# Optimization experiments

Measured on AMD Instinct MI355X. Metric: run time of the kernel, lower is better.

The kernel has to match this reference:

```python
import jax, jax.numpy as jnp
import numpy as np

EMB_DIM = 1024
N_HEADS = 16
HEAD_DIM = EMB_DIM // N_HEADS


def setup_inputs() -> dict:
    key = jax.random.key(0)
    ks = jax.random.split(key, 6)
    B, T, C = 2, 2048, EMB_DIM
    s = 1.0 / np.sqrt(C)
    return {
        "x": jax.random.normal(ks[0], (B, T, C), dtype=jnp.float32),
        "W_query": jax.random.normal(ks[1], (C, C), dtype=jnp.float32) * s,
        "W_key": jax.random.normal(ks[2], (C, C), dtype=jnp.float32) * s,
        "W_value": jax.random.normal(ks[3], (C, C), dtype=jnp.float32) * s,
        "W_out": jax.random.normal(ks[4], (C, C), dtype=jnp.float32) * s,
        "b_out": jax.random.normal(ks[5], (C,), dtype=jnp.float32) * 0.01,
    }


def reference(x, W_query, W_key, W_value, W_out, b_out):
    # x: [B, T, C]. Linear weights stored as [in, out] (transposed torch layout).
    B, T, C = x.shape
    H, D = N_HEADS, HEAD_DIM

    def split_heads(t):  # [B,T,C] -> [B,H,T,D]
        return t.reshape(B, T, H, D).transpose(0, 2, 1, 3)

    q = split_heads(x @ W_query)
    k = split_heads(x @ W_key)
    v = split_heads(x @ W_value)

    scale = 1.0 / jnp.sqrt(jnp.asarray(D, dtype=x.dtype))
    att = jnp.einsum("bhqd,bhkd->bhqk", q, k) * scale  # [B,H,T,T]
    causal = jnp.tril(jnp.ones((T, T), dtype=bool))
    att = jnp.where(causal[None, None], att, jnp.asarray(-jnp.inf, dtype=att.dtype))
    att = jax.nn.softmax(att, axis=-1)
    # dropout is identity in eval / drop_rate=0
    y = jnp.einsum("bhqk,bhkd->bhqd", att, v)  # [B,H,T,D]
    y = y.transpose(0, 2, 1, 3).reshape(B, T, C)
    return y @ W_out + b_out
```

## Files before the change

kernel.cpp:

```cpp
#include <hip/hip_runtime.h>
#include <hip/hip_bf16.h>
#include <math.h>

#define Bsz 2
#define Tsz 2048
#define Csz 1024
#define Hsz 16
#define Dsz 64

typedef __attribute__((ext_vector_type(8))) short frag8;
typedef __attribute__((ext_vector_type(4))) float f4;
typedef __attribute__((ext_vector_type(8))) unsigned short us8;

static __device__ __forceinline__ unsigned short f2bf(float f) {
  union { __hip_bfloat16 h; unsigned short u; } c;
  c.h = __float2bfloat16(f);
  return c.u;
}

#define GLDS16(g, l)                                                        \
  __builtin_amdgcn_global_load_lds(                                         \
      (const __attribute__((address_space(1))) void*)(g),                   \
      (__attribute__((address_space(3))) void*)(l), 16, 0, 0)

__global__ __launch_bounds__(256) void cast_x(const float* __restrict__ x,
                                              unsigned short* __restrict__ xb) {
  const int i = (blockIdx.x * 256 + threadIdx.x) * 8;
  const float4 a = *(const float4*)(x + i);
  const float4 b = *(const float4*)(x + i + 4);
  us8 v;
  v[0] = f2bf(a.x); v[1] = f2bf(a.y); v[2] = f2bf(a.z); v[3] = f2bf(a.w);
  v[4] = f2bf(b.x); v[5] = f2bf(b.y); v[6] = f2bf(b.z); v[7] = f2bf(b.w);
  *(us8*)(xb + i) = v;
}

__global__ __launch_bounds__(256) void transpose_cast(
    const float* __restrict__ s0, const float* __restrict__ s1,
    const float* __restrict__ s2, const float* __restrict__ s3,
    unsigned short* __restrict__ d0, unsigned short* __restrict__ d1,
    unsigned short* __restrict__ d2, unsigned short* __restrict__ d3) {
  __shared__ float Ls[64][65];
  const int mat = blockIdx.x >> 8;
  const int tile = blockIdx.x & 255;
  const float* src = mat == 0 ? s0 : mat == 1 ? s1 : mat == 2 ? s2 : s3;
  unsigned short* dst = mat == 0 ? d0 : mat == 1 ? d1 : mat == 2 ? d2 : d3;
  const int tr0 = (tile >> 4) << 6, tc0 = (tile & 15) << 6;
  const int t = threadIdx.x;
  const int lr = t >> 4, lc = (t & 15) << 2;
#pragma unroll
  for (int j = 0; j < 4; ++j) {
    const float4 v = *(const float4*)(src + (size_t)(tr0 + lr + j * 16) * 1024 + tc0 + lc);
    Ls[lr + j * 16][lc + 0] = v.x;
    Ls[lr + j * 16][lc + 1] = v.y;
    Ls[lr + j * 16][lc + 2] = v.z;
    Ls[lr + j * 16][lc + 3] = v.w;
  }
  __syncthreads();
#pragma unroll
  for (int j = 0; j < 4; ++j) {
    ushort4 v;
    v.x = f2bf(Ls[lc + 0][lr + j * 16]);
    v.y = f2bf(Ls[lc + 1][lr + j * 16]);
    v.z = f2bf(Ls[lc + 2][lr + j * 16]);
    v.w = f2bf(Ls[lc + 3][lr + j * 16]);
    *(ushort4*)(dst + (size_t)(tc0 + lr + j * 16) * 1024 + tr0 + lc) = v;
  }
}

template <int MODE>
__global__ __launch_bounds__(256) void mm_bt(
    const unsigned short* __restrict__ A, const unsigned short* __restrict__ Bt,
    const float* __restrict__ bias, unsigned short* __restrict__ O0,
    unsigned short* __restrict__ O1, unsigned short* __restrict__ O2,
    float* __restrict__ Of) {
  __shared__ __align__(16) unsigned short As[128 * 32];
  __shared__ __align__(16) unsigned short Bs[128 * 32];
  const int K = 1024;
  const int tid = threadIdx.x;
  const int wave = tid >> 6, lane = tid & 63;
  const int quad = lane >> 4, l16 = lane & 15;
  const int wm = wave >> 1, wn = wave & 1;
  const int row0 = blockIdx.y << 7, col0 = blockIdx.x << 7;

  const int sr = lane >> 2, sg = lane & 3;
  const int rA0 = wave * 32 + sr;
  const int g0 = sg ^ ((rA0 >> 1) & 3);
  const unsigned short* gA0 = A + (size_t)(row0 + rA0) * K + (g0 << 3);
  const unsigned short* gA1 = gA0 + (size_t)16 * K;
  const unsigned short* gB0 = Bt + (size_t)(col0 + rA0) * K + (g0 << 3);
  const unsigned short* gB1 = gB0 + (size_t)16 * K;
  unsigned short* lA0 = &As[(wave * 32) * 32];
  unsigned short* lA1 = &As[(wave * 32 + 16) * 32];
  unsigned short* lB0 = &Bs[(wave * 32) * 32];
  unsigned short* lB1 = &Bs[(wave * 32 + 16) * 32];

  f4 acc[4][4];
#pragma unroll
  for (int i = 0; i < 4; ++i)
#pragma unroll
    for (int j = 0; j < 4; ++j) acc[i][j] = (f4){0.f, 0.f, 0.f, 0.f};

  for (int kk = 0; kk < K; kk += 32) {
    __syncthreads();
    GLDS16(gA0 + kk, lA0);
    GLDS16(gA1 + kk, lA1);
    GLDS16(gB0 + kk, lB0);
    GLDS16(gB1 + kk, lB1);
    __syncthreads();

    frag8 af[4], bf[4];
#pragma unroll
    for (int mt = 0; mt < 4; ++mt) {
      const int r = wm * 64 + mt * 16 + l16;
      af[mt] = *(const frag8*)&As[r * 32 + ((quad ^ ((r >> 1) & 3)) << 3)];
    }
#pragma unroll
    for (int nt = 0; nt < 4; ++nt) {
      const int n = wn * 64 + nt * 16 + l16;
      bf[nt] = *(const frag8*)&Bs[n * 32 + ((quad ^ ((n >> 1) & 3)) << 3)];
    }
#pragma unroll
    for (int mt = 0; mt < 4; ++mt)
#pragma unroll
      for (int nt = 0; nt < 4; ++nt)
        acc[mt][nt] = __builtin_amdgcn_mfma_f32_16x16x32_bf16(af[mt], bf[nt], acc[mt][nt], 0, 0, 0);
  }

  if (MODE == 0) {
    if (col0 < 2048) {
      const bool isK = (col0 >= 1024);
      unsigned short* dst = isK ? O1 : O0;
      const float sc = isK ? 1.0f : 0.125f;
#pragma unroll
      for (int mt = 0; mt < 4; ++mt)
#pragma unroll
        for (int nt = 0; nt < 4; ++nt) {
          const int m = row0 + wm * 64 + mt * 16 + quad * 4;
          const int n = (col0 & 1023) + wn * 64 + nt * 16 + l16;
          const int b = m >> 11, h = n >> 6, d = n & 63;
#pragma unroll
          for (int r = 0; r < 4; ++r) {
            const int tk = (m + r) & (Tsz - 1);
            dst[(((size_t)b * Hsz + h) * Tsz + tk) * Dsz + d] = f2bf(acc[mt][nt][r] * sc);
          }
        }
    } else {
#pragma unroll
      for (int mt = 0; mt < 4; ++mt)
#pragma unroll
        for (int nt = 0; nt < 4; ++nt) {
          const int tok = row0 + wm * 64 + mt * 16 + quad * 4;
          const int ch = (col0 - 2048) + wn * 64 + nt * 16 + l16;
          const int b = tok >> 11, tk = tok & (Tsz - 1);
          const int h = ch >> 6, d = ch & 63;
          ushort4 v;
          v.x = f2bf(acc[mt][nt][0]); v.y = f2bf(acc[mt][nt][1]);
          v.z = f2bf(acc[mt][nt][2]); v.w = f2bf(acc[mt][nt][3]);
          *(ushort4*)&O2[(((size_t)b * Hsz + h) * Dsz + d) * Tsz + tk] = v;
        }
    }
  } else {
#pragma unroll
    for (int mt = 0; mt < 4; ++mt)
#pragma unroll
      for (int nt = 0; nt < 4; ++nt) {
        const int m = row0 + wm * 64 + mt * 16 + quad * 4;
        const int n = col0 + wn * 64 + nt * 16 + l16;
        const float bv = bias[n];
#pragma unroll
        for (int r = 0; r < 4; ++r)
          Of[(size_t)(m + r) * Csz + n] = acc[mt][nt][r] + bv;
      }
  }
}

#define PST 40
__global__ __launch_bounds__(256, 4) void attn_mfma(
    const unsigned short* __restrict__ Qb,
    const unsigned short* __restrict__ Kb,
    const unsigned short* __restrict__ VTb,
    unsigned short* __restrict__ Y) {
  __shared__ __align__(16) unsigned short Ks[2][2048];
  __shared__ __align__(16) unsigned short Vs[2][2048];
  __shared__ __align__(16) unsigned short Pb[4][16 * PST];

  const int tid = threadIdx.x;
  const int wave = tid >> 6, lane = tid & 63;
  const int quad = lane >> 4, l16 = lane & 15;

  const int bh = blockIdx.x >> 5;
  int qt = blockIdx.x & 31;
  if (bh >= 16) qt = 31 - qt;
  const int qb_w = (qt << 6) + wave * 16;

  const unsigned short* Qh = Qb + (size_t)bh * Tsz * Dsz;
  const unsigned short* Kh = Kb + (size_t)bh * Tsz * Dsz;
  const unsigned short* Vh = VTb + (size_t)bh * Dsz * Tsz;

  const int kkey = tid >> 3, kc = tid & 7;
  const int vd = tid >> 2, vc = tid & 3;
  const unsigned short* gK = Kh + (size_t)kkey * Dsz + ((kc ^ (kkey & 7)) << 3);
  const unsigned short* gV = Vh + (size_t)vd * Tsz + ((vc ^ ((vd + (vd >> 2)) & 3)) << 3);

  frag8 qf[2];
  qf[0] = *(const frag8*)(Qh + (size_t)(qb_w + l16) * Dsz + quad * 8);
  qf[1] = *(const frag8*)(Qh + (size_t)(qb_w + l16) * Dsz + 32 + quad * 8);

  f4 o[4];
  o[0] = o[1] = o[2] = o[3] = (f4){0.f, 0.f, 0.f, 0.f};
  float lsum = 0.f;
  const f4 zf = (f4){0.f, 0.f, 0.f, 0.f};
  unsigned short* Pw = &Pb[wave][0];
  const int fl = (l16 + (l16 >> 2)) & 3;
  const int kend_w = qb_w + 16;
  const int nch = 2 * qt + 2;

  GLDS16(gK, &Ks[0][wave * 512]);
  GLDS16(gV, &Vs[0][wave * 512]);
  GLDS16(gK + 32 * Dsz, &Ks[1][wave * 512]);
  GLDS16(gV + 32, &Vs[1][wave * 512]);
  __syncthreads();

  for (int i = 0; i < nch; ++i) {
    const int k0 = i << 5;
    const int bsel = i & 1;
    if (k0 < kend_w) {
      frag8 kf[2][2], vf[4];
#pragma unroll
      for (int n = 0; n < 2; ++n)
#pragma unroll
        for (int ks = 0; ks < 2; ++ks)
          kf[n][ks] = *(const frag8*)&Ks[bsel][(n * 16 + l16) * 64 + (((ks * 4 + quad) ^ (l16 & 7)) << 3)];
#pragma unroll
      for (int nt = 0; nt < 4; ++nt)
        vf[nt] = *(const frag8*)&Vs[bsel][(nt * 16 + l16) * 32 + ((quad ^ fl) << 3)];

      f4 st[2];
#pragma unroll
      for (int n = 0; n < 2; ++n) {
        f4 a = __builtin_amdgcn_mfma_f32_16x16x32_bf16(kf[n][0], qf[0], zf, 0, 0, 0);
        st[n] = __builtin_amdgcn_mfma_f32_16x16x32_bf16(kf[n][1], qf[1], a, 0, 0, 0);
      }

      const bool domask = (k0 + 31 > qb_w);
#pragma unroll
      for (int n = 0; n < 2; ++n) {
        const int key0 = k0 + n * 16 + quad * 4;
        ushort4 pk;
        float p0, p1, p2, p3;
        {
          float sv = st[n][0];
          if (domask && (key0 + 0 > qb_w + l16)) sv = -INFINITY;
          p0 = __expf(sv);
        }
        {
          float sv = st[n][1];
          if (domask && (key0 + 1 > qb_w + l16)) sv = -INFINITY;
          p1 = __expf(sv);
        }
        {
          float sv = st[n][2];
          if (domask && (key0 + 2 > qb_w + l16)) sv = -INFINITY;
          p2 = __expf(sv);
        }
        {
          float sv = st[n][3];
          if (domask && (key0 + 3 > qb_w + l16)) sv = -INFINITY;
          p3 = __expf(sv);
        }
        lsum += (p0 + p1) + (p2 + p3);
        pk.x = f2bf(p0); pk.y = f2bf(p1); pk.z = f2bf(p2); pk.w = f2bf(p3);
        *(ushort4*)&Pw[l16 * PST + n * 16 + quad * 4] = pk;
      }

      const frag8 pf = *(const frag8*)&Pw[l16 * PST + quad * 8];
#pragma unroll
      for (int nt = 0; nt < 4; ++nt)
        o[nt] = __builtin_amdgcn_mfma_f32_16x16x32_bf16(pf, vf[nt], o[nt], 0, 0, 0);
    }
    __syncthreads();
    if (i + 2 < nch) {
      GLDS16(gK + (size_t)(k0 + 64) * Dsz, &Ks[bsel][wave * 512]);
      GLDS16(gV + (k0 + 64), &Vs[bsel][wave * 512]);
    }
  }

  lsum += __shfl_xor(lsum, 16);
  lsum += __shfl_xor(lsum, 32);

  const int b = bh >> 4, h = bh & 15;
#pragma unroll
  for (int r = 0; r < 4; ++r) {
    const float inv = 1.f / __shfl(lsum, quad * 4 + r);
    const int t = qb_w + quad * 4 + r;
    unsigned short* yp = Y + ((size_t)b * Tsz + t) * Csz + h * 64 + l16;
#pragma unroll
    for (int nt = 0; nt < 4; ++nt)
      yp[nt * 16] = f2bf(o[nt][r] * inv);
  }
}

extern "C" void kernel_launch(void* const* d_in, const int* in_sizes, int n_in,
                              void* d_out, int out_size, void* d_ws, size_t ws_size,
                              hipStream_t stream) {
  const float* x  = (const float*)d_in[0];
  const float* Wq = (const float*)d_in[1];
  const float* Wk = (const float*)d_in[2];
  const float* Wv = (const float*)d_in[3];
  const float* Wo = (const float*)d_in[4];
  const float* bo = (const float*)d_in[5];

  const size_t NEL = (size_t)Bsz * Tsz * Csz;
  const size_t WSZ = (size_t)Csz * Csz;
  unsigned short* xb  = (unsigned short*)d_ws;
  unsigned short* WT  = xb + NEL;
  unsigned short* WoT = WT + 3 * WSZ;
  unsigned short* Qb  = WoT + WSZ;
  unsigned short* Kb  = Qb + NEL;
  unsigned short* VTb = Kb + NEL;
  unsigned short* Yb  = VTb + NEL;

  cast_x<<<NEL / 2048, 256, 0, stream>>>(x, xb);
  transpose_cast<<<1024, 256, 0, stream>>>(Wq, Wk, Wv, Wo,
                                           WT, WT + WSZ, WT + 2 * WSZ, WoT);

  mm_bt<0><<<dim3(24, 32), 256, 0, stream>>>(xb, WT, nullptr, Qb, Kb, VTb, nullptr);

  attn_mfma<<<Bsz * Hsz * (Tsz / 64), 256, 0, stream>>>(Qb, Kb, VTb, Yb);

  mm_bt<2><<<dim3(8, 32), 256, 0, stream>>>(Yb, WoT, bo, nullptr, nullptr, nullptr,
                                            (float*)d_out);
}
```

Baseline: 196.9 us.

## Retile GEMMs to K=64, widen attention to 32 rows per wave, fp16 PV via registers

The GEMM now stages K=64 slices with an 8-way XOR swizzle, and is templated on M tile so the output projection uses 64-row tiles for more blocks. Attention now handles 128 queries per block and 32 per wave, which reuses each K/V chunk across two query subtiles. It folds log2(e) into the Q scale and uses exp2, and stores V and P as fp16. When the 16x16x16 f16 MFMA is available, P feeds the PV MFMA straight from registers with no LDS round trip. Costs are higher register pressure, occupancy hint dropped to 2, fewer attention blocks, and fp16 range risk for V.

```diff
diff --git a/kernel.cpp b/kernel.cpp
--- a/kernel.cpp
+++ b/kernel.cpp
@@ -11,17 +11,30 @@
 typedef __attribute__((ext_vector_type(8))) short frag8;
 typedef __attribute__((ext_vector_type(4))) float f4;
 typedef __attribute__((ext_vector_type(8))) unsigned short us8;
+typedef __attribute__((ext_vector_type(4))) _Float16 frag4h;
+typedef __attribute__((ext_vector_type(8))) _Float16 frag8h;
+
+#if __has_builtin(__builtin_amdgcn_mfma_f32_16x16x16f16)
+#define PV_DIRECT 1
+#endif
 
 static __device__ __forceinline__ unsigned short f2bf(float f) {
   union { __hip_bfloat16 h; unsigned short u; } c;
   c.h = __float2bfloat16(f);
   return c.u;
 }
+static __device__ __forceinline__ unsigned short f2h(float f) {
+  union { _Float16 h; unsigned short u; } c;
+  c.h = (_Float16)f;
+  return c.u;
+}
 
 #define GLDS16(g, l)                                                        \
   __builtin_amdgcn_global_load_lds(                                         \
       (const __attribute__((address_space(1))) void*)(g),                   \
       (__attribute__((address_space(3))) void*)(l), 16, 0, 0)
+
+#define QSCALE 0.18033688f
 
 __global__ __launch_bounds__(256) void cast_x(const float* __restrict__ x,
                                               unsigned short* __restrict__ xb) {
@@ -67,75 +80,73 @@
   }
 }
 
-template <int MODE>
+template <int MODE, int MT>
 __global__ __launch_bounds__(256) void mm_bt(
     const unsigned short* __restrict__ A, const unsigned short* __restrict__ Bt,
     const float* __restrict__ bias, unsigned short* __restrict__ O0,
     unsigned short* __restrict__ O1, unsigned short* __restrict__ O2,
     float* __restrict__ Of) {
-  __shared__ __align__(16) unsigned short As[128 * 32];
-  __shared__ __align__(16) unsigned short Bs[128 * 32];
+  __shared__ __align__(16) unsigned short As[MT * 32 * 64];
+  __shared__ __align__(16) unsigned short Bs[128 * 64];
   const int K = 1024;
   const int tid = threadIdx.x;
   const int wave = tid >> 6, lane = tid & 63;
   const int quad = lane >> 4, l16 = lane & 15;
-  const int wm = wave >> 1, wn = wave & 1;
-  const int row0 = blockIdx.y << 7, col0 = blockIdx.x << 7;
-
-  const int sr = lane >> 2, sg = lane & 3;
-  const int rA0 = wave * 32 + sr;
-  const int g0 = sg ^ ((rA0 >> 1) & 3);
-  const unsigned short* gA0 = A + (size_t)(row0 + rA0) * K + (g0 << 3);
-  const unsigned short* gA1 = gA0 + (size_t)16 * K;
-  const unsigned short* gB0 = Bt + (size_t)(col0 + rA0) * K + (g0 << 3);
-  const unsigned short* gB1 = gB0 + (size_t)16 * K;
-  unsigned short* lA0 = &As[(wave * 32) * 32];
-  unsigned short* lA1 = &As[(wave * 32 + 16) * 32];
-  unsigned short* lB0 = &Bs[(wave * 32) * 32];
-  unsigned short* lB1 = &Bs[(wave * 32 + 16) * 32];
-
-  f4 acc[4][4];
-#pragma unroll
-  for (int i = 0; i < 4; ++i)
+  const int wrow = (wave >> 1) * (MT * 16), wn = wave & 1;
+  const int row0 = blockIdx.y * (MT * 32), col0 = blockIdx.x << 7;
+
+  const int sr = lane >> 3, sg = lane & 7;
+  const int g0 = sg ^ sr;
+  const unsigned short* gA = A + (size_t)(row0 + wave * (MT * 8) + sr) * K + (g0 << 3);
+  const unsigned short* gB = Bt + (size_t)(col0 + wave * 32 + sr) * K + (g0 << 3);
+
+  f4 acc[MT][4];
+#pragma unroll
+  for (int i = 0; i < MT; ++i)
 #pragma unroll
     for (int j = 0; j < 4; ++j) acc[i][j] = (f4){0.f, 0.f, 0.f, 0.f};
 
-  for (int kk = 0; kk < K; kk += 32) {
+  for (int kk = 0; kk < K; kk += 64) {
     __syncthreads();
-    GLDS16(gA0 + kk, lA0);
-    GLDS16(gA1 + kk, lA1);
-    GLDS16(gB0 + kk, lB0);
-    GLDS16(gB1 + kk, lB1);
+#pragma unroll
+    for (int s = 0; s < MT; ++s)
+      GLDS16(gA + kk + (size_t)(s * 8) * K, &As[(wave * (MT * 8) + s * 8) * 64]);
+#pragma unroll
+    for (int s = 0; s < 4; ++s)
+      GLDS16(gB + kk + (size_t)(s * 8) * K, &Bs[(wave * 32 + s * 8) * 64]);
     __syncthreads();
 
-    frag8 af[4], bf[4];
-#pragma unroll
-    for (int mt = 0; mt < 4; ++mt) {
-      const int r = wm * 64 + mt * 16 + l16;
-      af[mt] = *(const frag8*)&As[r * 32 + ((quad ^ ((r >> 1) & 3)) << 3)];
-    }
-#pragma unroll
-    for (int nt = 0; nt < 4; ++nt) {
-      const int n = wn * 64 + nt * 16 + l16;
-      bf[nt] = *(const frag8*)&Bs[n * 32 + ((quad ^ ((n >> 1) & 3)) << 3)];
-    }
-#pragma unroll
-    for (int mt = 0; mt < 4; ++mt)
-#pragma unroll
-      for (int nt = 0; nt < 4; ++nt)
-        acc[mt][nt] = __builtin_amdgcn_mfma_f32_16x16x32_bf16(af[mt], bf[nt], acc[mt][nt], 0, 0, 0);
+#pragma unroll
+    for (int ks = 0; ks < 2; ++ks) {
+      frag8 af[MT], bf[4];
+#pragma unroll
+      for (int mt = 0; mt < MT; ++mt) {
+        const int r = wrow + mt * 16 + l16;
+        af[mt] = *(const frag8*)&As[r * 64 + (((ks * 4 + quad) ^ (l16 & 7)) << 3)];
+      }
+#pragma unroll
+      for (int nt = 0; nt < 4; ++nt) {
+        const int n = wn * 64 + nt * 16 + l16;
+        bf[nt] = *(const frag8*)&Bs[n * 64 + (((ks * 4 + quad) ^ (l16 & 7)) << 3)];
+      }
+#pragma unroll
+      for (int mt = 0; mt < MT; ++mt)
+#pragma unroll
+        for (int nt = 0; nt < 4; ++nt)
+          acc[mt][nt] = __builtin_amdgcn_mfma_f32_16x16x32_bf16(af[mt], bf[nt], acc[mt][nt], 0, 0, 0);
+    }
   }
 
   if (MODE == 0) {
     if (col0 < 2048) {
       const bool isK = (col0 >= 1024);
       unsigned short* dst = isK ? O1 : O0;
-      const float sc = isK ? 1.0f : 0.125f;
-#pragma unroll
-      for (int mt = 0; mt < 4; ++mt)
+      const float sc = isK ? 1.0f : QSCALE;
+#pragma unroll
+      for (int mt = 0; mt < MT; ++mt)
 #pragma unroll
         for (int nt = 0; nt < 4; ++nt) {
-          const int m = row0 + wm * 64 + mt * 16 + quad * 4;
+          const int m = row0 + wrow + mt * 16 + quad * 4;
           const int n = (col0 & 1023) + wn * 64 + nt * 16 + l16;
           const int b = m >> 11, h = n >> 6, d = n & 63;
 #pragma unroll
@@ -146,25 +157,25 @@
         }
     } else {
 #pragma unroll
-      for (int mt = 0; mt < 4; ++mt)
+      for (int mt = 0; mt < MT; ++mt)
 #pragma unroll
         for (int nt = 0; nt < 4; ++nt) {
-          const int tok = row0 + wm * 64 + mt * 16 + quad * 4;
+          const int tok = row0 + wrow + mt * 16 + quad * 4;
           const int ch = (col0 - 2048) + wn * 64 + nt * 16 + l16;
           const int b = tok >> 11, tk = tok & (Tsz - 1);
           const int h = ch >> 6, d = ch & 63;
           ushort4 v;
-          v.x = f2bf(acc[mt][nt][0]); v.y = f2bf(acc[mt][nt][1]);
-          v.z = f2bf(acc[mt][nt][2]); v.w = f2bf(acc[mt][nt][3]);
+          v.x = f2h(acc[mt][nt][0]); v.y = f2h(acc[mt][nt][1]);
+          v.z = f2h(acc[mt][nt][2]); v.w = f2h(acc[mt][nt][3]);
           *(ushort4*)&O2[(((size_t)b * Hsz + h) * Dsz + d) * Tsz + tk] = v;
         }
     }
   } else {
 #pragma unroll
-    for (int mt = 0; mt < 4; ++mt)
+    for (int mt = 0; mt < MT; ++mt)
 #pragma unroll
       for (int nt = 0; nt < 4; ++nt) {
-        const int m = row0 + wm * 64 + mt * 16 + quad * 4;
+        const int m = row0 + wrow + mt * 16 + quad * 4;
         const int n = col0 + wn * 64 + nt * 16 + l16;
         const float bv = bias[n];
 #pragma unroll
@@ -174,24 +185,25 @@
   }
 }
 
-#define PST 40
-__global__ __launch_bounds__(256, 4) void attn_mfma(
+__global__ __launch_bounds__(256, 2) void attn_mfma(
     const unsigned short* __restrict__ Qb,
     const unsigned short* __restrict__ Kb,
     const unsigned short* __restrict__ VTb,
     unsigned short* __restrict__ Y) {
   __shared__ __align__(16) unsigned short Ks[2][2048];
   __shared__ __align__(16) unsigned short Vs[2][2048];
-  __shared__ __align__(16) unsigned short Pb[4][16 * PST];
-
+#ifndef PV_DIRECT
+  __shared__ __align__(16) unsigned short Pb[4][32 * 72];
+#endif
   const int tid = threadIdx.x;
   const int wave = tid >> 6, lane = tid & 63;
   const int quad = lane >> 4, l16 = lane & 15;
 
-  const int bh = blockIdx.x >> 5;
-  int qt = blockIdx.x & 31;
-  if (bh >= 16) qt = 31 - qt;
-  const int qb_w = (qt << 6) + wave * 16;
+  const int bh = blockIdx.x >> 4;
+  const int qtr = blockIdx.x & 15;
+  const int qt = (bh < 16) ? (15 - qtr) : qtr;
+  const int qb0 = qt << 7;
+  const int qb_w = qb0 + wave * 32;
 
   const unsigned short* Qh = Qb + (size_t)bh * Tsz * Dsz;
   const unsigned short* Kh = Kb + (size_t)bh * Tsz * Dsz;
@@ -202,22 +214,28 @@
   const unsigned short* gK = Kh + (size_t)kkey * Dsz + ((kc ^ (kkey & 7)) << 3);
   const unsigned short* gV = Vh + (size_t)vd * Tsz + ((vc ^ ((vd + (vd >> 2)) & 3)) << 3);
 
-  frag8 qf[2];
-  qf[0] = *(const frag8*)(Qh + (size_t)(qb_w + l16) * Dsz + quad * 8);
-  qf[1] = *(const frag8*)(Qh + (size_t)(qb_w + l16) * Dsz + 32 + quad * 8);
-
-  f4 o[4];
-  o[0] = o[1] = o[2] = o[3] = (f4){0.f, 0.f, 0.f, 0.f};
-  float lsum = 0.f;
+  frag8 qf[2][2];
+#pragma unroll
+  for (int m = 0; m < 2; ++m)
+#pragma unroll
+    for (int ks = 0; ks < 2; ++ks)
+      qf[m][ks] = *(const frag8*)(Qh + (size_t)(qb_w + m * 16 + l16) * Dsz + ks * 32 + quad * 8);
+
+  f4 o[2][4];
+  float lsum[2] = {0.f, 0.f};
+#pragma unroll
+  for (int m = 0; m < 2; ++m)
+#pragma unroll
+    for (int nt = 0; nt < 4; ++nt) o[m][nt] = (f4){0.f, 0.f, 0.f, 0.f};
+
   const f4 zf = (f4){0.f, 0.f, 0.f, 0.f};
-  unsigned short* Pw = &Pb[wave][0];
   const int fl = (l16 + (l16 >> 2)) & 3;
-  const int kend_w = qb_w + 16;
-  const int nch = 2 * qt + 2;
+  const int kend_w = qb_w + 32;
+  const int nch = (qb0 >> 5) + 4;
 
   GLDS16(gK, &Ks[0][wave * 512]);
   GLDS16(gV, &Vs[0][wave * 512]);
-  GLDS16(gK + 32 * Dsz, &Ks[1][wave * 512]);
+  GLDS16(gK + (size_t)32 * Dsz, &Ks[1][wave * 512]);
   GLDS16(gV + 32, &Vs[1][wave * 512]);
   __syncthreads();
 
@@ -225,58 +243,82 @@
     const int k0 = i << 5;
     const int bsel = i & 1;
     if (k0 < kend_w) {
-      frag8 kf[2][2], vf[4];
+      frag8 kf[2][2];
 #pragma unroll
       for (int n = 0; n < 2; ++n)
 #pragma unroll
         for (int ks = 0; ks < 2; ++ks)
           kf[n][ks] = *(const frag8*)&Ks[bsel][(n * 16 + l16) * 64 + (((ks * 4 + quad) ^ (l16 & 7)) << 3)];
+
+      f4 st[2][2];
+#pragma unroll
+      for (int n = 0; n < 2; ++n)
+#pragma unroll
+        for (int m = 0; m < 2; ++m) {
+          f4 a = __builtin_amdgcn_mfma_f32_16x16x32_bf16(kf[n][0], qf[m][0], zf, 0, 0, 0);
+          st[n][m] = __builtin_amdgcn_mfma_f32_16x16x32_bf16(kf[n][1], qf[m][1], a, 0, 0, 0);
+        }
+
+      const bool domask = (k0 + 31 > qb_w);
+      frag4h paf[2][2];
+#pragma unroll
+      for (int m = 0; m < 2; ++m) {
+        const int qv = qb_w + m * 16 + l16;
+#pragma unroll
+        for (int n = 0; n < 2; ++n) {
+          const int key0 = k0 + n * 16 + quad * 4;
+          float p[4];
+#pragma unroll
+          for (int r = 0; r < 4; ++r) {
+            float sv = st[n][m][r];
+            if (domask && (key0 + r > qv)) sv = -INFINITY;
+            p[r] = __builtin_amdgcn_exp2f(sv);
+          }
+          lsum[m] += (p[0] + p[1]) + (p[2] + p[3]);
+          frag4h ph;
+          ph[0] = (_Float16)p[0]; ph[1] = (_Float16)p[1];
+          ph[2] = (_Float16)p[2]; ph[3] = (_Float16)p[3];
+          paf[m][n] = ph;
+        }
+      }
+
+#ifdef PV_DIRECT
+      frag4h vf[2][4];
+#pragma unroll
+      for (int n = 0; n < 2; ++n)
+#pragma unroll
+        for (int nt = 0; nt < 4; ++nt) {
+          const int g = 2 * n + (quad >> 1);
+          vf[n][nt] = *(const frag4h*)&Vs[bsel][(nt * 16 + l16) * 32 + ((g ^ fl) << 3) + ((quad & 1) << 2)];
+        }
+#pragma unroll
+      for (int m = 0; m < 2; ++m)
+#pragma unroll
+        for (int nt = 0; nt < 4; ++nt) {
+          f4 a = __builtin_amdgcn_mfma_f32_16x16x16f16(paf[m][0], vf[0][nt], o[m][nt], 0, 0, 0);
+          o[m][nt] = __builtin_amdgcn_mfma_f32_16x16x16f16(paf[m][1], vf[1][nt], a, 0, 0, 0);
+        }
+#else
+      unsigned short* Pw = &Pb[wave][0];
+#pragma unroll
+      for (int m = 0; m < 2; ++m)
+#pragma unroll
+        for (int n = 0; n < 2; ++n)
+          *(frag4h*)&Pw[(m * 16 + l16) * 72 + n * 16 + quad * 4] = paf[m][n];
+      frag8h pfh[2];
+#pragma unroll
+      for (int m = 0; m < 2; ++m)
+        pfh[m] = *(const frag8h*)&Pw[(m * 16 + l16) * 72 + quad * 8];
+      frag8h vf8[4];
 #pragma unroll
       for (int nt = 0; nt < 4; ++nt)
-        vf[nt] = *(const frag8*)&Vs[bsel][(nt * 16 + l16) * 32 + ((quad ^ fl) << 3)];
-
-      f4 st[2];
-#pragma unroll
-      for (int n = 0; n < 2; ++n) {
-        f4 a = __builtin_amdgcn_mfma_f32_16x16x32_bf16(kf[n][0], qf[0], zf, 0, 0, 0);
-        st[n] = __builtin_amdgcn_mfma_f32_16x16x32_bf16(kf[n][1], qf[1], a, 0, 0, 0);
-      }
-
-      const bool domask = (k0 + 31 > qb_w);
-#pragma unroll
-      for (int n = 0; n < 2; ++n) {
-        const int key0 = k0 + n * 16 + quad * 4;
-        ushort4 pk;
-        float p0, p1, p2, p3;
-        {
-          float sv = st[n][0];
-          if (domask && (key0 + 0 > qb_w + l16)) sv = -INFINITY;
-          p0 = __expf(sv);
-        }
-        {
-          float sv = st[n][1];
-          if (domask && (key0 + 1 > qb_w + l16)) sv = -INFINITY;
-          p1 = __expf(sv);
-        }
-        {
-          float sv = st[n][2];
-          if (domask && (key0 + 2 > qb_w + l16)) sv = -INFINITY;
-          p2 = __expf(sv);
-        }
-        {
-          float sv = st[n][3];
-          if (domask && (key0 + 3 > qb_w + l16)) sv = -INFINITY;
-          p3 = __expf(sv);
-        }
-        lsum += (p0 + p1) + (p2 + p3);
-        pk.x = f2bf(p0); pk.y = f2bf(p1); pk.z = f2bf(p2); pk.w = f2bf(p3);
-        *(ushort4*)&Pw[l16 * PST + n * 16 + quad * 4] = pk;
-      }
-
-      const frag8 pf = *(const frag8*)&Pw[l16 * PST + quad * 8];
-#pragma unroll
-      for (int nt = 0; nt < 4; ++nt)
-        o[nt] = __builtin_amdgcn_mfma_f32_16x16x32_bf16(pf, vf[nt], o[nt], 0, 0, 0);
+        vf8[nt] = *(const frag8h*)&Vs[bsel][(nt * 16 + l16) * 32 + ((quad ^ fl) << 3)];
+#pragma unroll
+      for (int m = 0; m < 2; ++m)
+#pragma unroll
+        for (int nt = 0; nt < 4; ++nt)
+          o[m][nt] = __builtin_amdgcn_mfma_f32_16x16x32_f16(pfh[m], vf8[nt], o[m][nt], 0, 0, 0);
+#endif
     }
     __syncthreads();
     if (i + 2 < nch) {
@@ -285,19 +327,24 @@
     }
   }
 
-  lsum += __shfl_xor(lsum, 16);
-  lsum += __shfl_xor(lsum, 32);
+#pragma unroll
+  for (int m = 0; m < 2; ++m) {
+    lsum[m] += __shfl_xor(lsum[m], 16);
+    lsum[m] += __shfl_xor(lsum[m], 32);
+  }
 
   const int b = bh >> 4, h = bh & 15;
 #pragma unroll
-  for (int r = 0; r < 4; ++r) {
-    const float inv = 1.f / __shfl(lsum, quad * 4 + r);
-    const int t = qb_w + quad * 4 + r;
-    unsigned short* yp = Y + ((size_t)b * Tsz + t) * Csz + h * 64 + l16;
-#pragma unroll
-    for (int nt = 0; nt < 4; ++nt)
-      yp[nt * 16] = f2bf(o[nt][r] * inv);
-  }
+  for (int m = 0; m < 2; ++m)
+#pragma unroll
+    for (int r = 0; r < 4; ++r) {
+      const float inv = 1.f / __shfl(lsum[m], quad * 4 + r);
+      const int t = qb_w + m * 16 + quad * 4 + r;
+      unsigned short* yp = Y + ((size_t)b * Tsz + t) * Csz + h * 64 + l16;
+#pragma unroll
+      for (int nt = 0; nt < 4; ++nt)
+        yp[nt * 16] = f2bf(o[m][nt][r] * inv);
+    }
 }
 
 extern "C" void kernel_launch(void* const* d_in, const int* in_sizes, int n_in,
@@ -324,10 +371,10 @@
   transpose_cast<<<1024, 256, 0, stream>>>(Wq, Wk, Wv, Wo,
                                            WT, WT + WSZ, WT + 2 * WSZ, WoT);
 
-  mm_bt<0><<<dim3(24, 32), 256, 0, stream>>>(xb, WT, nullptr, Qb, Kb, VTb, nullptr);
-
-  attn_mfma<<<Bsz * Hsz * (Tsz / 64), 256, 0, stream>>>(Qb, Kb, VTb, Yb);
-
-  mm_bt<2><<<dim3(8, 32), 256, 0, stream>>>(Yb, WoT, bo, nullptr, nullptr, nullptr,
-                                            (float*)d_out);
-}
+  mm_bt<0, 4><<<dim3(24, 32), 256, 0, stream>>>(xb, WT, nullptr, Qb, Kb, VTb, nullptr);
+
+  attn_mfma<<<Bsz * Hsz * (Tsz / 128), 256, 0, stream>>>(Qb, Kb, VTb, Yb);
+
+  mm_bt<2, 2><<<dim3(8, 64), 256, 0, stream>>>(Yb, WoT, bo, nullptr, nullptr, nullptr,
+                                               (float*)d_out);
+}
```

After: 199.3 us. No clear change (+1.2%).
